# Kernel optimization log

Measured on AMD Instinct MI355X. Metric: run time of the kernel, lower is better.

Reference implementation:

```python
import jax, jax.numpy as jnp
import numpy as np

N = 4096
FIN = 256
FOUT = 256
H = 1  # num_heads MUST be 1: edge projections reshape [N,N,H] -> (1,N,N)
NEG_MASK = -1000000.0
LRELU_SLOPE = 0.2
ESP = 1e-06
LN_EPS = 1e-05


def setup_inputs() -> dict:
    key = jax.random.key(0)
    ks = jax.random.split(key, 9)
    nodes_features = jax.random.normal(ks[0], (N, FIN), dtype=jnp.float32)
    degree_matrix = jax.random.normal(ks[1], (N, N), dtype=jnp.float32)
    edges_features_distance = jax.random.uniform(ks[2], (N, N), dtype=jnp.float32)
    edges_features_bond = jax.random.uniform(ks[3], (N, N), dtype=jnp.float32)
    # learned parameters (xavier-ish scale)
    proj_param = jax.random.normal(ks[4], (H, FIN, FOUT), dtype=jnp.float32) * (1.0 / np.sqrt(FIN))
    a_src = jax.random.normal(ks[5], (H, FOUT, 1), dtype=jnp.float32) * (1.0 / np.sqrt(FOUT))
    a_tgt = jax.random.normal(ks[6], (H, FOUT, 1), dtype=jnp.float32) * (1.0 / np.sqrt(FOUT))
    w_dist = jax.random.normal(ks[7], (H, 1), dtype=jnp.float32)  # nn.Linear(1, H).weight
    w_bond = jax.random.normal(ks[8], (H, 1), dtype=jnp.float32)
    return {
        "nodes_features": nodes_features,
        "degree_matrix": degree_matrix,
        "edges_features_distance": edges_features_distance,
        "edges_features_bond": edges_features_bond,
        "proj_param": proj_param,
        "a_src": a_src,
        "a_tgt": a_tgt,
        "w_dist": w_dist,
        "w_bond": w_bond,
        "cutoff": 0,
    }


def reference(nodes_features, degree_matrix, edges_features_distance,
              edges_features_bond, proj_param, a_src, a_tgt, w_dist, w_bond,
              cutoff=0):
    n = nodes_features.shape[0]
    h, fin, fout = proj_param.shape
    # connectivity mask: keep degree where positive, else large negative
    connectivity_mask = jnp.where(degree_matrix > 0, degree_matrix, NEG_MASK)
    # node projection: [H, N, Fout] (dropout is identity in eval)
    proj = jnp.einsum('nf,hfo->hno', nodes_features, proj_param)
    # attention scores: outer-sum of per-node source/target scores
    s_src = jnp.einsum('hno,hoi->hni', proj, a_src)      # [H, N, 1]
    s_tgt = jnp.einsum('hno,hoi->hni', proj, a_tgt)      # [H, N, 1]
    all_scores = jax.nn.leaky_relu(s_src + jnp.swapaxes(s_tgt, 1, 2), LRELU_SLOPE)  # [H,N,N]
    # edge contributions: Linear(1, H) on scalar edge features, reshaped (1,N,N) (H==1)
    dist_c = ((-edges_features_distance)[..., None] * w_dist[:, 0]).reshape(1, n, n)
    bond_c = (edges_features_bond[..., None] * w_bond[:, 0]).reshape(1, n, n)
    all_scores = all_scores + dist_c + bond_c
    # masked softmax over neighbors
    attn = jax.nn.softmax(all_scores + connectivity_mask[None], axis=-1)  # [H,N,N]
    # weighted aggregation
    out = jnp.einsum('hnm,hmo->hno', attn, proj)  # [H, N, Fout]
    # faithful to torch: transpose(2,1) -> [H,Fout,N] then contiguous view(-1,H,Fout)
    out = jnp.transpose(out, (0, 2, 1)).reshape(-1, h, fout)
    # concat heads (skip connection and bias are disabled per init args)
    out = out.reshape(-1, h * fout)
    out = jax.nn.elu(out)  # ELU activation, alpha=1
    # ---- no_grad connectivity update ----
    o = jax.lax.stop_gradient(out)
    dm = jax.lax.stop_gradient(degree_matrix)
    sim = o @ o.T                                        # [N, N]
    decay = -jax.lax.stop_gradient(edges_features_distance)
    upd = jax.nn.sigmoid(sim) * decay * (dm > 0).astype(o.dtype)
    upd = upd + ESP
    mean = jnp.mean(upd, axis=-1, keepdims=True)
    var = jnp.mean(jnp.square(upd - mean), axis=-1, keepdims=True)
    upd = (upd - mean) / jnp.sqrt(var + LN_EPS)          # layer_norm, no affine
    upd = upd + upd.T
    return out, upd
```

## Files before the change

### kernel.cpp

```cpp
#include <hip/hip_runtime.h>


using f32x4  = __attribute__((ext_vector_type(4))) float;
using bf16x8 = __attribute__((ext_vector_type(8))) __bf16;
using bf16x4 = __attribute__((ext_vector_type(4))) __bf16;
using u32x4  = __attribute__((ext_vector_type(4))) unsigned int;

__global__ __launch_bounds__(256) void cvt_nodes_kernel(const float* __restrict__ x,
                                                        __bf16* __restrict__ y) {
  int i = (blockIdx.x * 256 + threadIdx.x) * 4;
  f32x4 v = *(const f32x4*)(x + i);
  bf16x4 o = { (__bf16)v[0], (__bf16)v[1], (__bf16)v[2], (__bf16)v[3] };
  *(bf16x4*)(y + i) = o;
}

__global__ __launch_bounds__(256) void cvt_wt_kernel(const float* __restrict__ w,
                                                     __bf16* __restrict__ wt) {
  int i = blockIdx.x * 256 + threadIdx.x;
  int o = i >> 8, f = i & 255;
  wt[i] = (__bf16)w[f * 256 + o];
}

__global__ __launch_bounds__(256) void zero_kernel(float* __restrict__ p) {
  p[blockIdx.x * 256 + threadIdx.x] = 0.0f;
}

template<int BM, int BN, int MODE>
__global__ __launch_bounds__(256) void gemm_bf16_kernel(
    const __bf16* __restrict__ A, const __bf16* __restrict__ Bt,
    int M, int N, int K,
    float* __restrict__ outf, __bf16* __restrict__ outb,
    const float* __restrict__ e0, const float* __restrict__ e1,
    const __bf16* __restrict__ axp, float* __restrict__ outt)
{
  constexpr int LDT = 72;
  constexpr int MI = BM / 32;
  constexpr int NI = BN / 32;
  __shared__ alignas(16) __bf16 As[BM * LDT];
  __shared__ alignas(16) __bf16 Bs[BN * LDT];
  const int tid  = threadIdx.x;
  const int lane = tid & 63;
  const int wid  = tid >> 6;
  const int wm0  = (wid >> 1) * (BM / 2);
  const int wn0  = (wid & 1) * (BN / 2);
  const int m0   = blockIdx.x * BM;
  const int n0   = blockIdx.y * BN;
  const int lr   = lane & 15;
  const int lk   = lane >> 4;

  f32x4 acc[MI][NI];
#pragma unroll
  for (int a = 0; a < MI; ++a)
#pragma unroll
    for (int b = 0; b < NI; ++b) acc[a][b] = (f32x4){0.f, 0.f, 0.f, 0.f};

  for (int kt = 0; kt < K; kt += 64) {
    __syncthreads();
    for (int idx = tid; idx < BM * 8; idx += 256) {
      int r = idx >> 3, c = idx & 7;
      u32x4 v = *(const u32x4*)(A + (size_t)(m0 + r) * K + kt + c * 8);
      *(u32x4*)(As + r * LDT + c * 8) = v;
    }
    for (int idx = tid; idx < BN * 8; idx += 256) {
      int r = idx >> 3, c = idx & 7;
      u32x4 v = *(const u32x4*)(Bt + (size_t)(n0 + r) * K + kt + c * 8);
      *(u32x4*)(Bs + r * LDT + c * 8) = v;
    }
    __syncthreads();
#pragma unroll
    for (int kk = 0; kk < 2; ++kk) {
      bf16x8 av[MI], bv[NI];
#pragma unroll
      for (int mi = 0; mi < MI; ++mi)
        av[mi] = *(const bf16x8*)(As + (wm0 + mi * 16 + lr) * LDT + kk * 32 + lk * 8);
#pragma unroll
      for (int ni = 0; ni < NI; ++ni)
        bv[ni] = *(const bf16x8*)(Bs + (wn0 + ni * 16 + lr) * LDT + kk * 32 + lk * 8);
#pragma unroll
      for (int mi = 0; mi < MI; ++mi)
#pragma unroll
        for (int ni = 0; ni < NI; ++ni)
          acc[mi][ni] = __builtin_amdgcn_mfma_f32_16x16x32_bf16(av[mi], bv[ni], acc[mi][ni], 0, 0, 0);
    }
  }

#pragma unroll
  for (int mi = 0; mi < MI; ++mi) {
#pragma unroll
    for (int ni = 0; ni < NI; ++ni) {
#pragma unroll
      for (int j = 0; j < 4; ++j) {
        const int m = m0 + wm0 + mi * 16 + lk * 4 + j;
        const int n = n0 + wn0 + ni * 16 + lr;
        const float v = acc[mi][ni][j];
        if constexpr (MODE == 0) {
          outf[(size_t)m * 256 + n] = v;
          outb[(size_t)n * 4096 + m] = (__bf16)v;
        } else if constexpr (MODE == 2) {
          const size_t idx = (size_t)m * 4096 + n;
          const float d = e0[idx];
          const float g = e1[idx];
          const float s = 1.0f / (1.0f + __expf(-v));
          outt[idx] = s * (-d) * (g > 0.f ? 1.0f : 0.0f) + 1e-6f;
        } else {
          const size_t idx = (size_t)m * 4096 + n;
          const float a = (float)axp[idx];
          const float s = 1.0f / (1.0f + __expf(-v));
          outt[idx] = s * a + 1e-6f;
        }
      }
    }
  }
}

__global__ __launch_bounds__(256) void score_exp_kernel(
    const float* __restrict__ dist, const float* __restrict__ bond,
    const float* __restrict__ deg,  const float* __restrict__ ssrc,
    const float* __restrict__ stgt, const float* __restrict__ wdp,
    const float* __restrict__ wbp,  __bf16* __restrict__ P,
    __bf16* __restrict__ aux,       float* __restrict__ Lrow)
{
  const float wd = wdp[0], wb = wbp[0];
  const int lane = threadIdx.x & 63;
  size_t i = ((size_t)blockIdx.x * 256 + threadIdx.x) * 4;
  const size_t stride = (size_t)2048 * 256 * 4;
#pragma unroll 2
  for (int it = 0; it < 8; ++it, i += stride) {
    const int row = (int)(i >> 12);
    const int col = (int)(i & 4095);
    f32x4 d  = __builtin_nontemporal_load((const f32x4*)(dist + i));
    f32x4 g  = __builtin_nontemporal_load((const f32x4*)(deg + i));
    f32x4 b  = __builtin_nontemporal_load((const f32x4*)(bond + i));
    f32x4 st = *(const f32x4*)(stgt + col);
    const float si = ssrc[row];
    f32x4 p;
    bf16x4 pb, ab;
#pragma unroll
    for (int q = 0; q < 4; ++q) {
      float x = si + st[q];
      x = x > 0.f ? x : 0.2f * x;
      x += -d[q] * wd + b[q] * wb + (g[q] > 0.f ? g[q] : -1000000.0f);
      p[q] = __expf(x);
      pb[q] = (__bf16)p[q];
      ab[q] = (__bf16)(g[q] > 0.f ? -d[q] : 0.0f);
    }
    *(bf16x4*)(P + i) = pb;
    if (aux) *(bf16x4*)(aux + i) = ab;
    float s = p[0] + p[1] + p[2] + p[3];
#pragma unroll
    for (int o = 32; o; o >>= 1) s += __shfl_xor(s, o, 64);
    if (lane == 0) atomicAdd(Lrow + row, s);
  }
}

__global__ __launch_bounds__(256) void gemm_splitk_kernel(
    const __bf16* __restrict__ A, const __bf16* __restrict__ Bt,
    __bf16* __restrict__ partial)
{
  constexpr int LDT = 72;
  __shared__ alignas(16) __bf16 As[64 * LDT];
  __shared__ alignas(16) __bf16 Bs[64 * LDT];
  const int tid  = threadIdx.x;
  const int lane = tid & 63;
  const int wid  = tid >> 6;
  const int wm0  = (wid >> 1) * 32;
  const int wn0  = (wid & 1) * 32;
  const int m0   = blockIdx.x * 64;
  const int n0   = blockIdx.y * 64;
  const int s    = blockIdx.z;
  const int lr   = lane & 15;
  const int lk   = lane >> 4;

  f32x4 acc[2][2];
#pragma unroll
  for (int a = 0; a < 2; ++a)
#pragma unroll
    for (int b = 0; b < 2; ++b) acc[a][b] = (f32x4){0.f, 0.f, 0.f, 0.f};

  const int k0 = s * 512;
  for (int kt = k0; kt < k0 + 512; kt += 64) {
    __syncthreads();
    for (int idx = tid; idx < 512; idx += 256) {
      int r = idx >> 3, c = idx & 7;
      u32x4 v = *(const u32x4*)(A + (size_t)(m0 + r) * 4096 + kt + c * 8);
      *(u32x4*)(As + r * LDT + c * 8) = v;
    }
    for (int idx = tid; idx < 512; idx += 256) {
      int r = idx >> 3, c = idx & 7;
      u32x4 v = *(const u32x4*)(Bt + (size_t)(n0 + r) * 4096 + kt + c * 8);
      *(u32x4*)(Bs + r * LDT + c * 8) = v;
    }
    __syncthreads();
#pragma unroll
    for (int kk = 0; kk < 2; ++kk) {
      bf16x8 av[2], bv[2];
#pragma unroll
      for (int mi = 0; mi < 2; ++mi)
        av[mi] = *(const bf16x8*)(As + (wm0 + mi * 16 + lr) * LDT + kk * 32 + lk * 8);
#pragma unroll
      for (int ni = 0; ni < 2; ++ni)
        bv[ni] = *(const bf16x8*)(Bs + (wn0 + ni * 16 + lr) * LDT + kk * 32 + lk * 8);
#pragma unroll
      for (int mi = 0; mi < 2; ++mi)
#pragma unroll
        for (int ni = 0; ni < 2; ++ni)
          acc[mi][ni] = __builtin_amdgcn_mfma_f32_16x16x32_bf16(av[mi], bv[ni], acc[mi][ni], 0, 0, 0);
    }
  }

  __bf16* Pp = partial + (size_t)s * (4096 * 256);
#pragma unroll
  for (int mi = 0; mi < 2; ++mi)
#pragma unroll
    for (int ni = 0; ni < 2; ++ni)
#pragma unroll
      for (int j = 0; j < 4; ++j) {
        const int m = m0 + wm0 + mi * 16 + lk * 4 + j;
        const int n = n0 + wn0 + ni * 16 + lr;
        Pp[(size_t)m * 256 + n] = (__bf16)acc[mi][ni][j];
      }
}

__global__ __launch_bounds__(256) void reduce_elu_kernel(
    const __bf16* __restrict__ partial, const float* __restrict__ Lrow,
    float* __restrict__ out0, __bf16* __restrict__ E)
{
  __shared__ float tile[64][65];
  __shared__ float invL[64];
  const int tid = threadIdx.x;
  const int m0 = blockIdx.x * 64;
  const int f0 = blockIdx.y * 64;
  if (tid < 64) invL[tid] = 1.0f / Lrow[m0 + tid];
  f32x4 accv[4];
#pragma unroll
  for (int i = 0; i < 4; ++i) {
    int lin = i * 1024 + tid * 4;
    int r = lin >> 6, c = lin & 63;
    f32x4 sum = (f32x4){0.f, 0.f, 0.f, 0.f};
#pragma unroll
    for (int s = 0; s < 8; ++s) {
      bf16x4 pv = *(const bf16x4*)(partial + (size_t)s * (4096 * 256) +
                                   (size_t)(m0 + r) * 256 + f0 + c);
#pragma unroll
      for (int q = 0; q < 4; ++q) sum[q] += (float)pv[q];
    }
    accv[i] = sum;
  }
  __syncthreads();
#pragma unroll
  for (int i = 0; i < 4; ++i) {
    int lin = i * 1024 + tid * 4;
    int r = lin >> 6, c = lin & 63;
    const float inv = invL[r];
    tile[r][c]     = accv[i][0] * inv;
    tile[r][c + 1] = accv[i][1] * inv;
    tile[r][c + 2] = accv[i][2] * inv;
    tile[r][c + 3] = accv[i][3] * inv;
  }
  __syncthreads();
#pragma unroll
  for (int i = 0; i < 4; ++i) {
    int lin = i * 1024 + tid * 4;
    int rr = lin >> 6, cc = lin & 63;
    f32x4 e;
#pragma unroll
    for (int q = 0; q < 4; ++q) {
      float v = tile[cc + q][rr];
      e[q] = v > 0.f ? v : expm1f(v);
    }
    size_t idx = (size_t)(f0 + rr) * 4096 + m0 + cc;
    *(f32x4*)(out0 + idx) = e;
    bf16x4 eb = { (__bf16)e[0], (__bf16)e[1], (__bf16)e[2], (__bf16)e[3] };
    *(bf16x4*)(E + idx) = eb;
  }
}

__global__ __launch_bounds__(256) void sproj_kernel(const float* __restrict__ proj,
                                                    const float* __restrict__ asrc,
                                                    const float* __restrict__ atgt,
                                                    float* __restrict__ ssrc,
                                                    float* __restrict__ stgt) {
  const int row  = blockIdx.x * 4 + (threadIdx.x >> 6);
  const int lane = threadIdx.x & 63;
  f32x4 p = *(const f32x4*)(proj + (size_t)row * 256 + lane * 4);
  f32x4 a = *(const f32x4*)(asrc + lane * 4);
  f32x4 b = *(const f32x4*)(atgt + lane * 4);
  float d1 = p[0]*a[0] + p[1]*a[1] + p[2]*a[2] + p[3]*a[3];
  float d2 = p[0]*b[0] + p[1]*b[1] + p[2]*b[2] + p[3]*b[3];
#pragma unroll
  for (int o = 32; o; o >>= 1) { d1 += __shfl_xor(d1, o, 64); d2 += __shfl_xor(d2, o, 64); }
  if (lane == 0) { ssrc[row] = d1; stgt[row] = d2; }
}

__global__ __launch_bounds__(256, 4) void stats_kernel(const float* __restrict__ t,
                                                       float* __restrict__ mean,
                                                       float* __restrict__ rstd) {
  const int row = blockIdx.x;
  const int tid = threadIdx.x;
  const float* tr = t + (size_t)row * 4096;
  f32x4 v[4];
#pragma unroll
  for (int u = 0; u < 4; ++u) v[u] = *(const f32x4*)(tr + u * 1024 + tid * 4);
  float s = 0.f, s2 = 0.f;
#pragma unroll
  for (int u = 0; u < 4; ++u)
#pragma unroll
    for (int q = 0; q < 4; ++q) { s += v[u][q]; s2 += v[u][q] * v[u][q]; }
#pragma unroll
  for (int o = 32; o; o >>= 1) { s += __shfl_xor(s, o, 64); s2 += __shfl_xor(s2, o, 64); }
  __shared__ float bs[4], bs2[4];
  if ((tid & 63) == 0) { bs[tid >> 6] = s; bs2[tid >> 6] = s2; }
  __syncthreads();
  if (tid == 0) {
    float S  = bs[0] + bs[1] + bs[2] + bs[3];
    float S2 = bs2[0] + bs2[1] + bs2[2] + bs2[3];
    float m  = S * (1.0f / 4096.0f);
    float var = S2 * (1.0f / 4096.0f) - m * m;
    mean[row] = m;
    rstd[row] = rsqrtf(var + 1e-5f);
  }
}

__global__ __launch_bounds__(256) void finalize_kernel(float* __restrict__ t,
                                                       const float* __restrict__ mean,
                                                       const float* __restrict__ rstd) {
  const int bj = blockIdx.x, bi = blockIdx.y;
  if (bi > bj) return;
  __shared__ float ta[64][65];
  __shared__ float tb[64][65];
  const int tid = threadIdx.x;
#pragma unroll
  for (int i = 0; i < 4; ++i) {
    int lin = i * 1024 + tid * 4;
    int r = lin >> 6, c = lin & 63;
    f32x4 va = *(const f32x4*)(t + (size_t)(bi * 64 + r) * 4096 + bj * 64 + c);
    ta[r][c] = va[0]; ta[r][c+1] = va[1]; ta[r][c+2] = va[2]; ta[r][c+3] = va[3];
  }
  if (bi != bj) {
#pragma unroll
    for (int i = 0; i < 4; ++i) {
      int lin = i * 1024 + tid * 4;
      int r = lin >> 6, c = lin & 63;
      f32x4 vb = *(const f32x4*)(t + (size_t)(bj * 64 + r) * 4096 + bi * 64 + c);
      tb[r][c] = vb[0]; tb[r][c+1] = vb[1]; tb[r][c+2] = vb[2]; tb[r][c+3] = vb[3];
    }
  }
  __syncthreads();
#pragma unroll
  for (int i = 0; i < 4; ++i) {
    int lin = i * 1024 + tid * 4;
    int r = lin >> 6, c = lin & 63;
    int gi = bi * 64 + r, gj = bj * 64 + c;
    const float mi_ = mean[gi], ri_ = rstd[gi];
    f32x4 mj = *(const f32x4*)(mean + gj);
    f32x4 rj = *(const f32x4*)(rstd + gj);
    f32x4 o;
#pragma unroll
    for (int q = 0; q < 4; ++q) {
      float v = (ta[r][c + q] - mi_) * ri_;
      float w = (bi == bj) ? (ta[c + q][r] - mj[q]) * rj[q]
                           : (tb[c + q][r] - mj[q]) * rj[q];
      o[q] = v + w;
    }
    *(f32x4*)(t + (size_t)gi * 4096 + gj) = o;
  }
  if (bi != bj) {
#pragma unroll
    for (int i = 0; i < 4; ++i) {
      int lin = i * 1024 + tid * 4;
      int r = lin >> 6, c = lin & 63;
      int gi = bj * 64 + r, gj = bi * 64 + c;
      const float mi_ = mean[gi], ri_ = rstd[gi];
      f32x4 mj = *(const f32x4*)(mean + gj);
      f32x4 rj = *(const f32x4*)(rstd + gj);
      f32x4 o;
#pragma unroll
      for (int q = 0; q < 4; ++q) {
        float v = (tb[r][c + q] - mi_) * ri_;
        float w = (ta[c + q][r] - mj[q]) * rj[q];
        o[q] = v + w;
      }
      *(f32x4*)(t + (size_t)gi * 4096 + gj) = o;
    }
  }
}

extern "C" void kernel_launch(void* const* d_in, const int* in_sizes, int n_in,
                              void* d_out, int out_size, void* d_ws, size_t ws_size,
                              hipStream_t stream) {
  const float* nodes  = (const float*)d_in[0];
  const float* degree = (const float*)d_in[1];
  const float* dist   = (const float*)d_in[2];
  const float* bond   = (const float*)d_in[3];
  const float* W      = (const float*)d_in[4];
  const float* a_src  = (const float*)d_in[5];
  const float* a_tgt  = (const float*)d_in[6];
  const float* w_dist = (const float*)d_in[7];
  const float* w_bond = (const float*)d_in[8];

  char* ws = (char*)d_ws;
  __bf16* nodesB = (__bf16*)ws;
  __bf16* Wt     = (__bf16*)(ws + (2u << 20));
  __bf16* projT  = (__bf16*)(ws + (2u << 20) + (256u << 10));
  float*  proj   = (float*)(ws + (5u << 20));
  __bf16* E      = (__bf16*)(ws + (9u << 20));
  float*  ssrc   = (float*)(ws + (11u << 20));
  float*  stgt   = ssrc + 4096;
  float*  mean   = stgt + 4096;
  float*  rstd   = mean + 4096;
  float*  Lrow   = rstd + 4096;

  const bool useAux = ws_size >= (size_t)(44u << 20);
  __bf16* aux = useAux ? (__bf16*)(ws + (12u << 20)) : nullptr;

  float*  out0 = (float*)d_out;
  float*  t    = out0 + (size_t)4096 * 256;
  __bf16* P    = (__bf16*)t;
  __bf16* partials = (__bf16*)((char*)t + ((size_t)32 << 20));

  cvt_nodes_kernel<<<1024, 256, 0, stream>>>(nodes, nodesB);
  cvt_wt_kernel<<<256, 256, 0, stream>>>(W, Wt);

  gemm_bf16_kernel<64, 64, 0><<<dim3(64, 4), 256, 0, stream>>>(
      nodesB, Wt, 4096, 256, 256, proj, projT, nullptr, nullptr, nullptr, nullptr);

  sproj_kernel<<<1024, 256, 0, stream>>>(proj, a_src, a_tgt, ssrc, stgt);

  zero_kernel<<<16, 256, 0, stream>>>(Lrow);

  score_exp_kernel<<<2048, 256, 0, stream>>>(dist, bond, degree, ssrc, stgt,
                                             w_dist, w_bond, P, aux, Lrow);

  gemm_splitk_kernel<<<dim3(64, 4, 8), 256, 0, stream>>>(P, projT, partials);

  reduce_elu_kernel<<<dim3(64, 4), 256, 0, stream>>>(partials, Lrow, out0, E);

  if (useAux)
    gemm_bf16_kernel<128, 128, 3><<<dim3(32, 32), 256, 0, stream>>>(
        E, E, 4096, 4096, 256, nullptr, nullptr, nullptr, nullptr, aux, t);
  else
    gemm_bf16_kernel<128, 128, 2><<<dim3(32, 32), 256, 0, stream>>>(
        E, E, 4096, 4096, 256, nullptr, nullptr, dist, degree, nullptr, t);

  stats_kernel<<<4096, 256, 0, stream>>>(t, mean, rstd);

  finalize_kernel<<<dim3(64, 64), 256, 0, stream>>>(t, mean, rstd);
}
```

Before: 180.8 us.

## Fuse layernorm row statistics into similarity GEMM epilogue and retile split-K GEMM

New measurement: 187.7 us. 3.8% more time.

```diff
diff --git a/kernel.cpp b/kernel.cpp
--- a/kernel.cpp
+++ b/kernel.cpp
@@ -31,7 +31,8 @@
     int M, int N, int K,
     float* __restrict__ outf, __bf16* __restrict__ outb,
     const float* __restrict__ e0, const float* __restrict__ e1,
-    const __bf16* __restrict__ axp, float* __restrict__ outt)
+    const __bf16* __restrict__ axp, float* __restrict__ outt,
+    float* __restrict__ bsum, float* __restrict__ bsq)
 {
   constexpr int LDT = 72;
   constexpr int MI = BM / 32;
@@ -84,33 +85,75 @@
     }
   }
 
-#pragma unroll
-  for (int mi = 0; mi < MI; ++mi) {
-#pragma unroll
-    for (int ni = 0; ni < NI; ++ni) {
+  if constexpr (MODE == 0) {
+#pragma unroll
+    for (int mi = 0; mi < MI; ++mi)
+#pragma unroll
+      for (int ni = 0; ni < NI; ++ni)
+#pragma unroll
+        for (int j = 0; j < 4; ++j) {
+          const int m = m0 + wm0 + mi * 16 + lk * 4 + j;
+          const int n = n0 + wn0 + ni * 16 + lr;
+          const float v = acc[mi][ni][j];
+          outf[(size_t)m * 256 + n] = v;
+          outb[(size_t)n * 4096 + m] = (__bf16)v;
+        }
+  } else {
+#pragma unroll
+    for (int mi = 0; mi < MI; ++mi) {
 #pragma unroll
       for (int j = 0; j < 4; ++j) {
         const int m = m0 + wm0 + mi * 16 + lk * 4 + j;
-        const int n = n0 + wn0 + ni * 16 + lr;
-        const float v = acc[mi][ni][j];
-        if constexpr (MODE == 0) {
-          outf[(size_t)m * 256 + n] = v;
-          outb[(size_t)n * 4096 + m] = (__bf16)v;
-        } else if constexpr (MODE == 2) {
+        float s = 0.f, s2 = 0.f;
+#pragma unroll
+        for (int ni = 0; ni < NI; ++ni) {
+          const int n = n0 + wn0 + ni * 16 + lr;
           const size_t idx = (size_t)m * 4096 + n;
-          const float d = e0[idx];
-          const float g = e1[idx];
-          const float s = 1.0f / (1.0f + __expf(-v));
-          outt[idx] = s * (-d) * (g > 0.f ? 1.0f : 0.0f) + 1e-6f;
-        } else {
-          const size_t idx = (size_t)m * 4096 + n;
-          const float a = (float)axp[idx];
-          const float s = 1.0f / (1.0f + __expf(-v));
-          outt[idx] = s * a + 1e-6f;
+          const float v = acc[mi][ni][j];
+          const float sg = 1.0f / (1.0f + __expf(-v));
+          float tval;
+          if constexpr (MODE == 2) {
+            const float d = e0[idx];
+            const float g = e1[idx];
+            tval = sg * (-d) * (g > 0.f ? 1.0f : 0.0f) + 1e-6f;
+          } else {
+            const float a = (float)__builtin_nontemporal_load(axp + idx);
+            tval = sg * a + 1e-6f;
+          }
+          outt[idx] = tval;
+          s += tval;
+          s2 += tval * tval;
+        }
+#pragma unroll
+        for (int o = 1; o < 16; o <<= 1) {
+          s  += __shfl_xor(s, o, 64);
+          s2 += __shfl_xor(s2, o, 64);
+        }
+        if (lr == 0) {
+          const int slot = blockIdx.y * 2 + (wid & 1);
+          bsum[(size_t)slot * 4096 + m] = s;
+          bsq [(size_t)slot * 4096 + m] = s2;
         }
       }
     }
   }
+}
+
+__global__ __launch_bounds__(256) void stats_small_kernel(
+    const float* __restrict__ bsum, const float* __restrict__ bsq,
+    float* __restrict__ mean, float* __restrict__ rstd)
+{
+  const int row = blockIdx.x * 256 + threadIdx.x;
+  float S = 0.f, S2 = 0.f;
+#pragma unroll 8
+  for (int s = 0; s < 64; ++s) {
+    S  += bsum[(size_t)s * 4096 + row];
+    S2 += bsq [(size_t)s * 4096 + row];
+  }
+  const float m  = S * (1.0f / 4096.0f);
+  const float var = S2 * (1.0f / 4096.0f) - m * m;
+  mean[row] = m;
+  rstd[row] = rsqrtf(var + 1e-5f);
 }
 
 __global__ __launch_bounds__(256) void score_exp_kernel(
@@ -123,9 +166,9 @@
   const float wd = wdp[0], wb = wbp[0];
   const int lane = threadIdx.x & 63;
   size_t i = ((size_t)blockIdx.x * 256 + threadIdx.x) * 4;
-  const size_t stride = (size_t)2048 * 256 * 4;
+  const size_t stride = (size_t)4096 * 256 * 4;
 #pragma unroll 2
-  for (int it = 0; it < 8; ++it, i += stride) {
+  for (int it = 0; it < 4; ++it, i += stride) {
     const int row = (int)(i >> 12);
     const int col = (int)(i & 4095);
     f32x4 d  = __builtin_nontemporal_load((const f32x4*)(dist + i));
@@ -159,23 +202,23 @@
 {
   constexpr int LDT = 72;
   __shared__ alignas(16) __bf16 As[64 * LDT];
-  __shared__ alignas(16) __bf16 Bs[64 * LDT];
+  __shared__ alignas(16) __bf16 Bs[128 * LDT];
   const int tid  = threadIdx.x;
   const int lane = tid & 63;
   const int wid  = tid >> 6;
   const int wm0  = (wid >> 1) * 32;
-  const int wn0  = (wid & 1) * 32;
+  const int wn0  = (wid & 1) * 64;
   const int m0   = blockIdx.x * 64;
-  const int n0   = blockIdx.y * 64;
+  const int n0   = blockIdx.y * 128;
   const int s    = blockIdx.z;
   const int lr   = lane & 15;
   const int lk   = lane >> 4;
 
-  f32x4 acc[2][2];
+  f32x4 acc[2][4];
 #pragma unroll
   for (int a = 0; a < 2; ++a)
 #pragma unroll
-    for (int b = 0; b < 2; ++b) acc[a][b] = (f32x4){0.f, 0.f, 0.f, 0.f};
+    for (int b = 0; b < 4; ++b) acc[a][b] = (f32x4){0.f, 0.f, 0.f, 0.f};
 
   const int k0 = s * 512;
   for (int kt = k0; kt < k0 + 512; kt += 64) {
@@ -185,7 +228,7 @@
       u32x4 v = *(const u32x4*)(A + (size_t)(m0 + r) * 4096 + kt + c * 8);
       *(u32x4*)(As + r * LDT + c * 8) = v;
     }
-    for (int idx = tid; idx < 512; idx += 256) {
+    for (int idx = tid; idx < 1024; idx += 256) {
       int r = idx >> 3, c = idx & 7;
       u32x4 v = *(const u32x4*)(Bt + (size_t)(n0 + r) * 4096 + kt + c * 8);
       *(u32x4*)(Bs + r * LDT + c * 8) = v;
@@ -193,17 +236,17 @@
     __syncthreads();
 #pragma unroll
     for (int kk = 0; kk < 2; ++kk) {
-      bf16x8 av[2], bv[2];
+      bf16x8 av[2], bv[4];
 #pragma unroll
       for (int mi = 0; mi < 2; ++mi)
         av[mi] = *(const bf16x8*)(As + (wm0 + mi * 16 + lr) * LDT + kk * 32 + lk * 8);
 #pragma unroll
-      for (int ni = 0; ni < 2; ++ni)
+      for (int ni = 0; ni < 4; ++ni)
         bv[ni] = *(const bf16x8*)(Bs + (wn0 + ni * 16 + lr) * LDT + kk * 32 + lk * 8);
 #pragma unroll
       for (int mi = 0; mi < 2; ++mi)
 #pragma unroll
-        for (int ni = 0; ni < 2; ++ni)
+        for (int ni = 0; ni < 4; ++ni)
           acc[mi][ni] = __builtin_amdgcn_mfma_f32_16x16x32_bf16(av[mi], bv[ni], acc[mi][ni], 0, 0, 0);
     }
   }
@@ -212,7 +255,7 @@
 #pragma unroll
   for (int mi = 0; mi < 2; ++mi)
 #pragma unroll
-    for (int ni = 0; ni < 2; ++ni)
+    for (int ni = 0; ni < 4; ++ni)
 #pragma unroll
       for (int j = 0; j < 4; ++j) {
         const int m = m0 + wm0 + mi * 16 + lk * 4 + j;
@@ -239,8 +282,9 @@
     f32x4 sum = (f32x4){0.f, 0.f, 0.f, 0.f};
 #pragma unroll
     for (int s = 0; s < 8; ++s) {
-      bf16x4 pv = *(const bf16x4*)(partial + (size_t)s * (4096 * 256) +
-                                   (size_t)(m0 + r) * 256 + f0 + c);
+      bf16x4 pv = __builtin_nontemporal_load(
+          (const bf16x4*)(partial + (size_t)s * (4096 * 256) +
+                          (size_t)(m0 + r) * 256 + f0 + c));
 #pragma unroll
       for (int q = 0; q < 4; ++q) sum[q] += (float)pv[q];
     }
@@ -269,7 +313,7 @@
       e[q] = v > 0.f ? v : expm1f(v);
     }
     size_t idx = (size_t)(f0 + rr) * 4096 + m0 + cc;
-    *(f32x4*)(out0 + idx) = e;
+    __builtin_nontemporal_store(e, (f32x4*)(out0 + idx));
     bf16x4 eb = { (__bf16)e[0], (__bf16)e[1], (__bf16)e[2], (__bf16)e[3] };
     *(bf16x4*)(E + idx) = eb;
   }
@@ -292,35 +336,6 @@
   if (lane == 0) { ssrc[row] = d1; stgt[row] = d2; }
 }
 
-__global__ __launch_bounds__(256, 4) void stats_kernel(const float* __restrict__ t,
-                                                       float* __restrict__ mean,
-                                                       float* __restrict__ rstd) {
-  const int row = blockIdx.x;
-  const int tid = threadIdx.x;
-  const float* tr = t + (size_t)row * 4096;
-  f32x4 v[4];
-#pragma unroll
-  for (int u = 0; u < 4; ++u) v[u] = *(const f32x4*)(tr + u * 1024 + tid * 4);
-  float s = 0.f, s2 = 0.f;
-#pragma unroll
-  for (int u = 0; u < 4; ++u)
-#pragma unroll
-    for (int q = 0; q < 4; ++q) { s += v[u][q]; s2 += v[u][q] * v[u][q]; }
-#pragma unroll
-  for (int o = 32; o; o >>= 1) { s += __shfl_xor(s, o, 64); s2 += __shfl_xor(s2, o, 64); }
-  __shared__ float bs[4], bs2[4];
-  if ((tid & 63) == 0) { bs[tid >> 6] = s; bs2[tid >> 6] = s2; }
-  __syncthreads();
-  if (tid == 0) {
-    float S  = bs[0] + bs[1] + bs[2] + bs[3];
-    float S2 = bs2[0] + bs2[1] + bs2[2] + bs2[3];
-    float m  = S * (1.0f / 4096.0f);
-    float var = S2 * (1.0f / 4096.0f) - m * m;
-    mean[row] = m;
-    rstd[row] = rsqrtf(var + 1e-5f);
-  }
-}
-
 __global__ __launch_bounds__(256) void finalize_kernel(float* __restrict__ t,
                                                        const float* __restrict__ mean,
                                                        const float* __restrict__ rstd) {
@@ -333,7 +348,8 @@
   for (int i = 0; i < 4; ++i) {
     int lin = i * 1024 + tid * 4;
     int r = lin >> 6, c = lin & 63;
-    f32x4 va = *(const f32x4*)(t + (size_t)(bi * 64 + r) * 4096 + bj * 64 + c);
+    f32x4 va = __builtin_nontemporal_load(
+        (const f32x4*)(t + (size_t)(bi * 64 + r) * 4096 + bj * 64 + c));
     ta[r][c] = va[0]; ta[r][c+1] = va[1]; ta[r][c+2] = va[2]; ta[r][c+3] = va[3];
   }
   if (bi != bj) {
@@ -341,7 +357,8 @@
     for (int i = 0; i < 4; ++i) {
       int lin = i * 1024 + tid * 4;
       int r = lin >> 6, c = lin & 63;
-      f32x4 vb = *(const f32x4*)(t + (size_t)(bj * 64 + r) * 4096 + bi * 64 + c);
+      f32x4 vb = __builtin_nontemporal_load(
+          (const f32x4*)(t + (size_t)(bj * 64 + r) * 4096 + bi * 64 + c));
       tb[r][c] = vb[0]; tb[r][c+1] = vb[1]; tb[r][c+2] = vb[2]; tb[r][c+3] = vb[3];
     }
   }
@@ -362,7 +379,7 @@
                            : (tb[c + q][r] - mj[q]) * rj[q];
       o[q] = v + w;
     }
-    *(f32x4*)(t + (size_t)gi * 4096 + gj) = o;
+    __builtin_nontemporal_store(o, (f32x4*)(t + (size_t)gi * 4096 + gj));
   }
   if (bi != bj) {
 #pragma unroll
@@ -380,7 +397,7 @@
         float w = (ta[c + q][r] - mj[q]) * rj[q];
         o[q] = v + w;
       }
-      *(f32x4*)(t + (size_t)gi * 4096 + gj) = o;
+      __builtin_nontemporal_store(o, (f32x4*)(t + (size_t)gi * 4096 + gj));
     }
   }
 }
@@ -410,8 +427,11 @@
   float*  rstd   = mean + 4096;
   float*  Lrow   = rstd + 4096;
 
-  const bool useAux = ws_size >= (size_t)(44u << 20);
-  __bf16* aux = useAux ? (__bf16*)(ws + (12u << 20)) : nullptr;
+  const bool useAux = ws_size >= (size_t)(48u << 20);
+  __bf16* aux  = useAux ? (__bf16*)(ws + (12u << 20)) : nullptr;
+  float* Bsum  = useAux ? (float*)(ws + (44u << 20))
+                        : (float*)(ws + (12u << 20));
+  float* Bsq   = Bsum + (size_t)64 * 4096;
 
   float*  out0 = (float*)d_out;
   float*  t    = out0 + (size_t)4096 * 256;
@@ -422,27 +442,30 @@
   cvt_wt_kernel<<<256, 256, 0, stream>>>(W, Wt);
 
   gemm_bf16_kernel<64, 64, 0><<<dim3(64, 4), 256, 0, stream>>>(
-      nodesB, Wt, 4096, 256, 256, proj, projT, nullptr, nullptr, nullptr, nullptr);
+      nodesB, Wt, 4096, 256, 256, proj, projT,
+      nullptr, nullptr, nullptr, nullptr, nullptr, nullptr);
 
   sproj_kernel<<<1024, 256, 0, stream>>>(proj, a_src, a_tgt, ssrc, stgt);
 
   zero_kernel<<<16, 256, 0, stream>>>(Lrow);
 
-  score_exp_kernel<<<2048, 256, 0, stream>>>(dist, bond, degree, ssrc, stgt,
+  score_exp_kernel<<<4096, 256, 0, stream>>>(dist, bond, degree, ssrc, stgt,
                                              w_dist, w_bond, P, aux, Lrow);
 
-  gemm_splitk_kernel<<<dim3(64, 4, 8), 256, 0, stream>>>(P, projT, partials);
+  gemm_splitk_kernel<<<dim3(64, 2, 8), 256, 0, stream>>>(P, projT, partials);
 
   reduce_elu_kernel<<<dim3(64, 4), 256, 0, stream>>>(partials, Lrow, out0, E);
 
   if (useAux)
     gemm_bf16_kernel<128, 128, 3><<<dim3(32, 32), 256, 0, stream>>>(
-        E, E, 4096, 4096, 256, nullptr, nullptr, nullptr, nullptr, aux, t);
+        E, E, 4096, 4096, 256, nullptr, nullptr,
+        nullptr, nullptr, aux, t, Bsum, Bsq);
   else
     gemm_bf16_kernel<128, 128, 2><<<dim3(32, 32), 256, 0, stream>>>(
-        E, E, 4096, 4096, 256, nullptr, nullptr, dist, degree, nullptr, t);
-
-  stats_kernel<<<4096, 256, 0, stream>>>(t, mean, rstd);
+        E, E, 4096, 4096, 256, nullptr, nullptr,
+        dist, degree, nullptr, t, Bsum, Bsq);
+
+  stats_small_kernel<<<16, 256, 0, stream>>>(Bsum, Bsq, mean, rstd);
 
   finalize_kernel<<<dim3(64, 64), 256, 0, stream>>>(t, mean, rstd);
 }
```
